# Optimization experiments

Measured on AMD Instinct MI355X. Metric: run time of the kernel, lower is better.

## Reference

```python
import jax, jax.numpy as jnp
import numpy as np

B, C = 4096, 10000
TAU = 1.0
MIN_K, MAX_K = 30, 100


def setup_inputs() -> dict:
    key = jax.random.key(0)
    k1, k2 = jax.random.split(key, 2)
    logit = jax.random.normal(k1, (B, C), dtype=jnp.float32)
    target = jax.random.randint(k2, (B,), 0, C)
    # long-tailed class counts: exponential decay from 1000 down to 5
    cls_num = np.exp(np.linspace(np.log(1000.0), np.log(5.0), C)).astype(np.float32)
    cls_num_ratio = cls_num / cls_num.sum()
    log_cls_num = jnp.asarray(np.log(cls_num_ratio + 1e-6), dtype=jnp.float32)
    freq = (cls_num.max() / cls_num).astype(np.float32)
    freq_norm = (freq - freq.min()) / (freq.max() - freq.min() + 1e-6)
    k_per_class = jnp.asarray((freq_norm * (MAX_K - MIN_K) + MIN_K).astype(np.int32))
    return {"logit": logit, "target": target, "log_cls_num": log_cls_num,
            "k_per_class": k_per_class}


def reference(logit, target, log_cls_num, k_per_class):
    b, c = logit.shape
    rows = jnp.arange(b)
    # logit-adjusted cross entropy (loss_full)
    logit_adj = logit + TAU * log_cls_num[None, :]
    log_p_adj = jax.nn.log_softmax(logit_adj, axis=1)  # [B, C]
    loss_full = -jnp.mean(log_p_adj[rows, target])
    # per-row variable-k top-k mask on the ORIGINAL logits
    prob_adj = jnp.exp(log_p_adj)
    k = jnp.minimum(k_per_class[target], c)            # [B]
    sorted_desc = -jnp.sort(-logit, axis=1)            # [B, C] descending
    thresh = sorted_desc[rows, k - 1]                  # k-th largest per row
    mask = logit >= thresh[:, None]
    masked_prob = jnp.where(mask, prob_adj, 0.0) + 1e-6
    masked_prob = masked_prob / masked_prob.sum(axis=1, keepdims=True)
    loss_topk = -jnp.mean(jnp.log(masked_prob)[rows, target])
    return 0.5 * loss_full + 0.5 * loss_topk
```

## Files before the change

### kernel.cpp

```cpp
#include <hip/hip_runtime.h>

#define BLOCK 256
#define C_DIM 10000
#define C4 (C_DIM / 4)
#define NIT ((C4 + BLOCK - 1) / BLOCK)
#define TAU 1.0f
#define PIV 2.0f
#define CAP 1024

__device__ __forceinline__ unsigned flip_key(float f) {
    unsigned u = __float_as_uint(f);
    return (u & 0x80000000u) ? ~u : (u | 0x80000000u);
}
__device__ __forceinline__ float unflip_key(unsigned k) {
    unsigned u = (k & 0x80000000u) ? (k & 0x7fffffffu) : ~k;
    return __uint_as_float(u);
}

__global__ void zero_out_kernel(float* out, int n) {
    int i = blockIdx.x * blockDim.x + threadIdx.x;
    if (i < n) out[i] = 0.f;
}

__device__ __forceinline__ void scan_pick(unsigned* hist, int shift, int tid,
                                          unsigned* shp, unsigned* shkr, unsigned* shcnt) {
    unsigned h0 = hist[4 * tid + 0], h1 = hist[4 * tid + 1];
    unsigned h2 = hist[4 * tid + 2], h3 = hist[4 * tid + 3];
    unsigned loc = h0 + h1 + h2 + h3;
    unsigned suf = loc;
    for (int off = 1; off < 64; off <<= 1) {
        unsigned o = __shfl_down(suf, off);
        if (tid + off < 64) suf += o;
    }
    unsigned sufex = suf - loc;
    unsigned kr = *shkr;
    unsigned s3 = sufex + h3;
    unsigned s2 = s3 + h2;
    unsigned s1 = s2 + h1;
    unsigned s0 = s1 + h0;
    int bsel = -1; unsigned newkr = 0, newcnt = 0;
    if      (s3 >= kr && s3 - h3 < kr) { bsel = 4 * tid + 3; newkr = kr - (s3 - h3); newcnt = h3; }
    else if (s2 >= kr && s2 - h2 < kr) { bsel = 4 * tid + 2; newkr = kr - (s2 - h2); newcnt = h2; }
    else if (s1 >= kr && s1 - h1 < kr) { bsel = 4 * tid + 1; newkr = kr - (s1 - h1); newcnt = h1; }
    else if (s0 >= kr && s0 - h0 < kr) { bsel = 4 * tid + 0; newkr = kr - (s0 - h0); newcnt = h0; }
    if (bsel >= 0) {
        *shp |= ((unsigned)bsel << shift);
        *shkr = newkr;
        *shcnt = newcnt;
    }
}

#define PROC4(f, l, j4)                                                              \
    {                                                                                \
        float a0 = (f).x + TAU * (l).x, a1 = (f).y + TAU * (l).y;                    \
        float a2 = (f).z + TAU * (l).z, a3 = (f).w + TAU * (l).w;                    \
        z0 += __expf(a0); z1 += __expf(a1); z2 += __expf(a2); z3 += __expf(a3);      \
        madj = fmaxf(madj, fmaxf(fmaxf(a0, a1), fmaxf(a2, a3)));                     \
        const int _pj = 4 * (j4);                                                    \
        if ((f).x >= PIV) { unsigned i = atomicAdd(&sh_nc, 1u); if (i < CAP) { candk[i] = __float_as_uint((f).x); candi[i] = (unsigned short)(_pj + 0); } } \
        if ((f).y >= PIV) { unsigned i = atomicAdd(&sh_nc, 1u); if (i < CAP) { candk[i] = __float_as_uint((f).y); candi[i] = (unsigned short)(_pj + 1); } } \
        if ((f).z >= PIV) { unsigned i = atomicAdd(&sh_nc, 1u); if (i < CAP) { candk[i] = __float_as_uint((f).z); candi[i] = (unsigned short)(_pj + 2); } } \
        if ((f).w >= PIV) { unsigned i = atomicAdd(&sh_nc, 1u); if (i < CAP) { candk[i] = __float_as_uint((f).w); candi[i] = (unsigned short)(_pj + 3); } } \
    }

__global__ __launch_bounds__(BLOCK, 8) void topk_la_loss_kernel(
    const float* __restrict__ logit, const int* __restrict__ target,
    const float* __restrict__ lcn, const int* __restrict__ kpc,
    float* __restrict__ out, int B) {
    __shared__ unsigned candk[CAP];
    __shared__ unsigned short candi[CAP];
    __shared__ unsigned hist[256];
    __shared__ float red_a[4], red_b[4];
    __shared__ unsigned sh_nc, sh_prefix, sh_kr, sh_cnt;
    __shared__ float sh_thresh, sh_Z, sh_madj;

    const int row = blockIdx.x;
    const int tid = threadIdx.x;
    const int lane = tid & 63;
    const int wid = tid >> 6;
    const float* lrow = logit + (size_t)row * C_DIM;

    const int t = target[row];
    int k = kpc[t]; if (k > C_DIM) k = C_DIM;

    if (tid == 0) sh_nc = 0u;
    __syncthreads();

    float z0 = 0.f, z1 = 0.f, z2 = 0.f, z3 = 0.f, madj = -INFINITY;
    const float4* lr4 = (const float4*)lrow;
    const float4* lc4 = (const float4*)lcn;
    for (int it = 0; it < 4; ++it) {
        int ja = it * (2 * BLOCK) + tid;
        int jb = ja + BLOCK;
        float4 fa = lr4[ja];
        float4 fb = lr4[jb];
        float4 la = lc4[ja];
        float4 lb = lc4[jb];
        PROC4(fa, la, ja);
        PROC4(fb, lb, jb);
    }
    {
        int j = 2048 + tid;
        float4 f = lr4[j];
        float4 l = lc4[j];
        PROC4(f, l, j);
    }
    if (tid < C4 - 2304) {
        int j = 2304 + tid;
        float4 f = lr4[j];
        float4 l = lc4[j];
        PROC4(f, l, j);
    }

    float z = (z0 + z1) + (z2 + z3);
    for (int off = 32; off; off >>= 1) {
        z += __shfl_down(z, off);
        madj = fmaxf(madj, __shfl_down(madj, off));
    }
    if (lane == 0) { red_a[wid] = z; red_b[wid] = madj; }
    __syncthreads();

    if (tid == 0) {
        sh_Z = red_a[0] + red_a[1] + red_a[2] + red_a[3];
        sh_madj = fmaxf(fmaxf(red_b[0], red_b[1]), fmaxf(red_b[2], red_b[3]));
        sh_prefix = 0u;
        sh_kr = (unsigned)k;
        sh_cnt = sh_nc;
    }
    __syncthreads();

    const unsigned nc = sh_nc;
    const float madjB = sh_madj;
    const bool rare = fabsf(madjB) > 80.f;
    const bool normal = (!rare) && (nc >= (unsigned)k) && (nc <= (unsigned)CAP);

    float sm = 0.f, zloc = 0.f;

    if (normal) {
        unsigned kmask = 0u;
        for (int q = 0; q < 4; ++q) {
            if (sh_cnt == 1u) break;
            const int shift = 24 - 8 * q;
            hist[tid] = 0u;
            __syncthreads();
            const unsigned pref = sh_prefix;
            for (int i = tid; i < (int)nc; i += BLOCK) {
                unsigned kk = candk[i];
                if ((kk & kmask) == pref) atomicAdd(&hist[(kk >> shift) & 0xFFu], 1u);
            }
            __syncthreads();
            if (tid < 64) scan_pick(hist, shift, tid, &sh_prefix, &sh_kr, &sh_cnt);
            kmask |= (0xFFu << shift);
            __syncthreads();
        }
        if (sh_cnt == 1u && kmask != 0xFFFFFFFFu) {
            const unsigned pref = sh_prefix;
            __syncthreads();
            for (int i = tid; i < (int)nc; i += BLOCK) {
                unsigned kk = candk[i];
                if ((kk & kmask) == pref) sh_prefix = kk;
            }
            __syncthreads();
        }
        if (tid == 0) sh_thresh = __uint_as_float(sh_prefix);
        __syncthreads();

        const float thresh = sh_thresh;
        for (int i = tid; i < (int)nc; i += BLOCK) {
            float v = __uint_as_float(candk[i]);
            if (v >= thresh) sm += __expf(v + TAU * lcn[candi[i]]);
        }
    } else {
        for (int p = 0; p < 4; ++p) {
            const int shift = 24 - 8 * p;
            const unsigned pmask = p ? (0xFFFFFFFFu << (shift + 8)) : 0u;
            hist[tid] = 0u;
            __syncthreads();
            const unsigned pref = sh_prefix;
            for (int it = 0; it < NIT; ++it) {
                int j4 = it * BLOCK + tid;
                if (j4 < C4) {
                    float4 f = lr4[j4];
                    unsigned kk;
                    kk = flip_key(f.x); if ((kk & pmask) == pref) atomicAdd(&hist[(kk >> shift) & 0xFFu], 1u);
                    kk = flip_key(f.y); if ((kk & pmask) == pref) atomicAdd(&hist[(kk >> shift) & 0xFFu], 1u);
                    kk = flip_key(f.z); if ((kk & pmask) == pref) atomicAdd(&hist[(kk >> shift) & 0xFFu], 1u);
                    kk = flip_key(f.w); if ((kk & pmask) == pref) atomicAdd(&hist[(kk >> shift) & 0xFFu], 1u);
                }
            }
            __syncthreads();
            if (tid < 64) scan_pick(hist, shift, tid, &sh_prefix, &sh_kr, &sh_cnt);
            __syncthreads();
        }
        if (tid == 0) sh_thresh = unflip_key(sh_prefix);
        __syncthreads();

        const float thresh = sh_thresh;
        const float sub = rare ? madjB : 0.f;
        for (int it = 0; it < NIT; ++it) {
            int j4 = it * BLOCK + tid;
            if (j4 < C4) {
                float4 f = lr4[j4];
                float4 l = lc4[j4];
                float e;
                e = __expf(f.x + TAU * l.x - sub); zloc += e; if (f.x >= thresh) sm += e;
                e = __expf(f.y + TAU * l.y - sub); zloc += e; if (f.y >= thresh) sm += e;
                e = __expf(f.z + TAU * l.z - sub); zloc += e; if (f.z >= thresh) sm += e;
                e = __expf(f.w + TAU * l.w - sub); zloc += e; if (f.w >= thresh) sm += e;
            }
        }
    }

    for (int off = 32; off; off >>= 1) {
        sm   += __shfl_down(sm, off);
        zloc += __shfl_down(zloc, off);
    }
    if (lane == 0) { red_a[wid] = zloc; red_b[wid] = sm; }
    __syncthreads();

    if (tid == 0) {
        float S  = red_b[0] + red_b[1] + red_b[2] + red_b[3];
        float Zu = normal ? sh_Z : (red_a[0] + red_a[1] + red_a[2] + red_a[3]);
        float thresh = sh_thresh;
        float logit_t = lrow[t];
        float adj_t = logit_t + TAU * lcn[t];
        float sub = rare ? madjB : 0.f;
        float lpt = adj_t - sub - __logf(Zu);
        float p_num = ((logit_t >= thresh) ? __expf(lpt) : 0.f) + 1e-6f;
        float Smask = S / Zu + (float)C_DIM * 1e-6f;
        float loss = 0.5f * (-lpt + __logf(Smask) - __logf(p_num));
        atomicAdd(out, loss / (float)B);
    }
}

extern "C" void kernel_launch(void* const* d_in, const int* in_sizes, int n_in,
                              void* d_out, int out_size, void* d_ws, size_t ws_size,
                              hipStream_t stream) {
    const float* logit  = (const float*)d_in[0];
    const int*   target = (const int*)d_in[1];
    const float* lcn    = (const float*)d_in[2];
    const int*   kpc    = (const int*)d_in[3];
    float* out = (float*)d_out;
    const int B = in_sizes[1];

    zero_out_kernel<<<1, 64, 0, stream>>>(out, out_size);
    topk_la_loss_kernel<<<B, BLOCK, 0, stream>>>(logit, target, lcn, kpc, out, B);
}
```

Before: 278.5 us.

## Split candidate collection into a second pass and store adjusted logits

Candidate gathering moves out of the first streaming loop into a separate pass that re-reads the row after the softmax reduction, so the first pass no longer carries shared-memory atomics. Candidates now store the already adjusted logit instead of a class index, which removes the lcn gather in the final sum. The cost is a second global read of each row and of lcn, which should mostly hit in cache, plus one fewer barrier at the start.

```diff
diff --git a/kernel.cpp b/kernel.cpp
--- a/kernel.cpp
+++ b/kernel.cpp
@@ -50,17 +50,20 @@
     }
 }
 
-#define PROC4(f, l, j4)                                                              \
+#define PROCZ(f, l)                                                                  \
     {                                                                                \
         float a0 = (f).x + TAU * (l).x, a1 = (f).y + TAU * (l).y;                    \
         float a2 = (f).z + TAU * (l).z, a3 = (f).w + TAU * (l).w;                    \
         z0 += __expf(a0); z1 += __expf(a1); z2 += __expf(a2); z3 += __expf(a3);      \
         madj = fmaxf(madj, fmaxf(fmaxf(a0, a1), fmaxf(a2, a3)));                     \
-        const int _pj = 4 * (j4);                                                    \
-        if ((f).x >= PIV) { unsigned i = atomicAdd(&sh_nc, 1u); if (i < CAP) { candk[i] = __float_as_uint((f).x); candi[i] = (unsigned short)(_pj + 0); } } \
-        if ((f).y >= PIV) { unsigned i = atomicAdd(&sh_nc, 1u); if (i < CAP) { candk[i] = __float_as_uint((f).y); candi[i] = (unsigned short)(_pj + 1); } } \
-        if ((f).z >= PIV) { unsigned i = atomicAdd(&sh_nc, 1u); if (i < CAP) { candk[i] = __float_as_uint((f).z); candi[i] = (unsigned short)(_pj + 2); } } \
-        if ((f).w >= PIV) { unsigned i = atomicAdd(&sh_nc, 1u); if (i < CAP) { candk[i] = __float_as_uint((f).w); candi[i] = (unsigned short)(_pj + 3); } } \
+    }
+
+#define APPEND4(f, l)                                                                \
+    {                                                                                \
+        if ((f).x >= PIV) { unsigned i = atomicAdd(&sh_nc, 1u); if (i < CAP) { candk[i] = __float_as_uint((f).x); canda[i] = (f).x + TAU * (l).x; } } \
+        if ((f).y >= PIV) { unsigned i = atomicAdd(&sh_nc, 1u); if (i < CAP) { candk[i] = __float_as_uint((f).y); canda[i] = (f).y + TAU * (l).y; } } \
+        if ((f).z >= PIV) { unsigned i = atomicAdd(&sh_nc, 1u); if (i < CAP) { candk[i] = __float_as_uint((f).z); canda[i] = (f).z + TAU * (l).z; } } \
+        if ((f).w >= PIV) { unsigned i = atomicAdd(&sh_nc, 1u); if (i < CAP) { candk[i] = __float_as_uint((f).w); canda[i] = (f).w + TAU * (l).w; } } \
     }
 
 __global__ __launch_bounds__(BLOCK, 8) void topk_la_loss_kernel(
@@ -68,7 +71,7 @@
     const float* __restrict__ lcn, const int* __restrict__ kpc,
     float* __restrict__ out, int B) {
     __shared__ unsigned candk[CAP];
-    __shared__ unsigned short candi[CAP];
+    __shared__ float canda[CAP];
     __shared__ unsigned hist[256];
     __shared__ float red_a[4], red_b[4];
     __shared__ unsigned sh_nc, sh_prefix, sh_kr, sh_cnt;
@@ -82,9 +85,6 @@
 
     const int t = target[row];
     int k = kpc[t]; if (k > C_DIM) k = C_DIM;
-
-    if (tid == 0) sh_nc = 0u;
-    __syncthreads();
 
     float z0 = 0.f, z1 = 0.f, z2 = 0.f, z3 = 0.f, madj = -INFINITY;
     const float4* lr4 = (const float4*)lrow;
@@ -96,20 +96,20 @@
         float4 fb = lr4[jb];
         float4 la = lc4[ja];
         float4 lb = lc4[jb];
-        PROC4(fa, la, ja);
-        PROC4(fb, lb, jb);
+        PROCZ(fa, la);
+        PROCZ(fb, lb);
     }
     {
         int j = 2048 + tid;
         float4 f = lr4[j];
         float4 l = lc4[j];
-        PROC4(f, l, j);
+        PROCZ(f, l);
     }
     if (tid < C4 - 2304) {
         int j = 2304 + tid;
         float4 f = lr4[j];
         float4 l = lc4[j];
-        PROC4(f, l, j);
+        PROCZ(f, l);
     }
 
     float z = (z0 + z1) + (z2 + z3);
@@ -123,10 +123,20 @@
     if (tid == 0) {
         sh_Z = red_a[0] + red_a[1] + red_a[2] + red_a[3];
         sh_madj = fmaxf(fmaxf(red_b[0], red_b[1]), fmaxf(red_b[2], red_b[3]));
-        sh_prefix = 0u;
-        sh_kr = (unsigned)k;
-        sh_cnt = sh_nc;
-    }
+        sh_nc = 0u;
+    }
+    __syncthreads();
+
+    for (int it = 0; it < NIT; ++it) {
+        int j4 = it * BLOCK + tid;
+        if (j4 < C4) {
+            float4 f = lr4[j4];
+            float4 l = lc4[j4];
+            APPEND4(f, l);
+        }
+    }
+    __syncthreads();
+    if (tid == 0) { sh_prefix = 0u; sh_kr = (unsigned)k; sh_cnt = sh_nc; }
     __syncthreads();
 
     const unsigned nc = sh_nc;
@@ -167,8 +177,7 @@
 
         const float thresh = sh_thresh;
         for (int i = tid; i < (int)nc; i += BLOCK) {
-            float v = __uint_as_float(candk[i]);
-            if (v >= thresh) sm += __expf(v + TAU * lcn[candi[i]]);
+            if (__uint_as_float(candk[i]) >= thresh) sm += __expf(canda[i]);
         }
     } else {
         for (int p = 0; p < 4; ++p) {
```

After: 292.8 us. +5.1%, slower.
